# Performance work log

Measured on AMD Instinct MI355X. Metric: run time of the kernel, lower is better.

The kernel has to match this reference:

```python
import jax, jax.numpy as jnp
import numpy as np

NUM_NODES = 2048
NODE_DIM = 64
BATCH = 16


def setup_inputs() -> dict:
    key = jax.random.key(0)
    ks = jax.random.split(key, 8)
    s = 1.0 / np.sqrt(NODE_DIM)
    return {
        "x_temp": jax.random.normal(ks[0], (BATCH, NUM_NODES, NODE_DIM), jnp.float32),
        "node_emb": jax.random.normal(ks[1], (NUM_NODES, NODE_DIM), jnp.float32),
        "w1_w": jax.random.uniform(ks[2], (NODE_DIM, NODE_DIM), jnp.float32, -s, s),
        "w1_b": jax.random.uniform(ks[3], (NODE_DIM,), jnp.float32, -s, s),
        "w2_w": jax.random.uniform(ks[4], (NODE_DIM, NODE_DIM), jnp.float32, -s, s),
        "w2_b": jax.random.uniform(ks[5], (NODE_DIM,), jnp.float32, -s, s),
        "wp_w": jax.random.uniform(ks[6], (1, NODE_DIM), jnp.float32, -s, s),
        "wp_b": jax.random.uniform(ks[7], (1,), jnp.float32, -s, s),
    }


def reference(x_temp, node_emb, w1_w, w1_b, w2_w, w2_b, wp_w, wp_b):
    # static bilinear adjacency over learned node embeddings: [N, N]
    node_1 = node_emb @ w1_w.T + w1_b
    node_2 = node_emb @ w2_w.T + w2_b
    adj_base = jax.nn.relu(node_1 @ node_2.T)
    # dynamic similarity from temporal states: [B, N, N]
    dyn = jnp.einsum("bnd,bmd->bnm", x_temp, x_temp)
    # directional (wind-like) antisymmetric bias: v_i - v_j
    v = x_temp @ wp_w.T + wp_b  # [B, N, 1]
    directional_bias = v - jnp.swapaxes(v, 1, 2)  # [B, N, N]
    adj = adj_base[None, :, :] + dyn + directional_bias
    return jax.nn.softmax(adj, axis=-1)
```

## Files before the change

### kernel.cpp

```cpp
#include <hip/hip_runtime.h>

#define BB 16
#define NN 2048
#define DD 64
#define MC 128
#define NCH (NN / MC)
#define TM 8

#define FW 8
#define FT 16


typedef __bf16 bf16x8 __attribute__((ext_vector_type(8)));
typedef float f32x4 __attribute__((ext_vector_type(4)));
typedef int i32x4 __attribute__((ext_vector_type(4)));
typedef unsigned short u16x8 __attribute__((ext_vector_type(8)));

#define MFMA16 __builtin_amdgcn_mfma_f32_16x16x32_bf16

__device__ inline unsigned short f2bf(float f) {
  unsigned u = __float_as_uint(f);
  unsigned r = u + 0x7FFFu + ((u >> 16) & 1u);
  return (unsigned short)(r >> 16);
}
__device__ inline float bf2f(unsigned short h) {
  return __uint_as_float(((unsigned)h) << 16);
}
__device__ inline bf16x8 ldfrag(const unsigned short* p) {
  i32x4 v = *reinterpret_cast<const i32x4*>(p);
  return __builtin_bit_cast(bf16x8, v);
}

__global__ __launch_bounds__(256) void prep_nodes(
    const float* __restrict__ emb, const float* __restrict__ w1w,
    const float* __restrict__ w1b, const float* __restrict__ w2w,
    const float* __restrict__ w2b, float* __restrict__ n1f,
    float* __restrict__ n2f, unsigned short* __restrict__ n1hi,
    unsigned short* __restrict__ n1lo, unsigned short* __restrict__ n2hi,
    unsigned short* __restrict__ n2lo, int wantbf)
{
  __shared__ float wl[2][DD][DD + 1];
  int t = threadIdx.x;
  for (int i = t; i < DD * DD; i += 256) {
    wl[0][i >> 6][i & 63] = w1w[i];
    wl[1][i >> 6][i & 63] = w2w[i];
  }
  __syncthreads();
  int g = blockIdx.x * 256 + t;
  int which = (g >= NN * DD) ? 1 : 0;
  int idx = which ? g - NN * DD : g;
  int n = idx >> 6, d = idx & 63;
  const float* e = emb + (size_t)n * DD;
  float s = which ? w2b[d] : w1b[d];
  #pragma unroll
  for (int k = 0; k < DD; ++k) s += e[k] * wl[which][d][k];
  (which ? n2f : n1f)[idx] = s;
  if (wantbf) {
    unsigned short hi = f2bf(s);
    unsigned short lo = f2bf(s - bf2f(hi));
    int ti = (n >> 4) * 1024 + (d >> 3) * 128 + (n & 15) * 8 + (d & 7);
    (which ? n2hi : n1hi)[ti] = hi;
    (which ? n2lo : n1lo)[ti] = lo;
  }
}

__global__ __launch_bounds__(256) void prep_x(
    const float* __restrict__ x, unsigned short* __restrict__ xhi,
    unsigned short* __restrict__ xlo)
{
  int G = blockIdx.x * 256 + threadIdx.x;
  int b = G >> 14;
  int rem = G & 16383;
  int tile = rem >> 7, oct = (rem >> 4) & 7, m = rem & 15;
  const float* src = x + ((size_t)b * NN + tile * 16 + m) * DD + oct * 8;
  float4 x0 = *(const float4*)src;
  float4 x1 = *(const float4*)(src + 4);
  u16x8 hv, lv;
  hv[0] = f2bf(x0.x); lv[0] = f2bf(x0.x - bf2f(hv[0]));
  hv[1] = f2bf(x0.y); lv[1] = f2bf(x0.y - bf2f(hv[1]));
  hv[2] = f2bf(x0.z); lv[2] = f2bf(x0.z - bf2f(hv[2]));
  hv[3] = f2bf(x0.w); lv[3] = f2bf(x0.w - bf2f(hv[3]));
  hv[4] = f2bf(x1.x); lv[4] = f2bf(x1.x - bf2f(hv[4]));
  hv[5] = f2bf(x1.y); lv[5] = f2bf(x1.y - bf2f(hv[5]));
  hv[6] = f2bf(x1.z); lv[6] = f2bf(x1.z - bf2f(hv[6]));
  hv[7] = f2bf(x1.w); lv[7] = f2bf(x1.w - bf2f(hv[7]));
  *(u16x8*)&xhi[(size_t)G * 8] = hv;
  *(u16x8*)&xlo[(size_t)G * 8] = lv;
}

__global__ __launch_bounds__(256) void prep_v(
    const float* __restrict__ x, const float* __restrict__ wpw,
    const float* __restrict__ wpb, float* __restrict__ v)
{
  int g = blockIdx.x * 256 + threadIdx.x;
  const float* xr = x + (size_t)g * DD;
  float s = wpb[0];
  #pragma unroll
  for (int kq = 0; kq < DD / 4; ++kq) {
    float4 q = *(const float4*)&xr[kq * 4];
    float4 w = *(const float4*)&wpw[kq * 4];
    s += q.x * w.x + q.y * w.y + q.z * w.z + q.w * w.w;
  }
  v[g] = s;
}

__global__ __launch_bounds__(256) void base_mfma(
    const unsigned short* __restrict__ n1hi, const unsigned short* __restrict__ n1lo,
    const unsigned short* __restrict__ n2hi, const unsigned short* __restrict__ n2lo,
    float* __restrict__ base)
{
  int t = threadIdx.x, lane = t & 63, w = t >> 6;
  int q = lane >> 4, m = lane & 15;
  int n0 = blockIdx.x * 16;
  int cw = blockIdx.y * 256 + w * 64;
  int la8 = lane * 8;
  bf16x8 ah0 = ldfrag(n1hi + n0 * 64 + la8), ah1 = ldfrag(n1hi + n0 * 64 + 512 + la8);
  bf16x8 al0 = ldfrag(n1lo + n0 * 64 + la8), al1 = ldfrag(n1lo + n0 * 64 + 512 + la8);
  #pragma unroll
  for (int tt = 0; tt < 4; ++tt) {
    int c0 = cw + tt * 16;
    bf16x8 bh0 = ldfrag(n2hi + c0 * 64 + la8), bh1 = ldfrag(n2hi + c0 * 64 + 512 + la8);
    bf16x8 bl0 = ldfrag(n2lo + c0 * 64 + la8), bl1 = ldfrag(n2lo + c0 * 64 + 512 + la8);
    f32x4 a = {0.f, 0.f, 0.f, 0.f};
    f32x4 bq = {0.f, 0.f, 0.f, 0.f};
    a = MFMA16(ah0, bh0, a, 0, 0, 0);
    a = MFMA16(ah1, bh1, a, 0, 0, 0);
    bq = MFMA16(ah0, bl0, bq, 0, 0, 0);
    bq = MFMA16(ah1, bl1, bq, 0, 0, 0);
    bq = MFMA16(al0, bh0, bq, 0, 0, 0);
    bq = MFMA16(al1, bh1, bq, 0, 0, 0);
    #pragma unroll
    for (int r = 0; r < 4; ++r)
      base[(size_t)(n0 + q * 4 + r) * NN + c0 + m] = fmaxf(a[r] + bq[r], 0.f);
  }
}

__global__ __launch_bounds__(512, 4) void fused_mfma(
    const unsigned short* __restrict__ xhi, const unsigned short* __restrict__ xlo,
    const float* __restrict__ base, const float* __restrict__ vv,
    float* __restrict__ out)
{
  __shared__ float redm[FW][16];
  __shared__ float reds[FW][16];
  int t = threadIdx.x, lane = t & 63, w = t >> 6;
  int q = lane >> 4, m = lane & 15;
  int b = blockIdx.y, n0 = blockIdx.x * 16, cw = w * (FT * 16);
  size_t xb = (size_t)b * NN * DD;
  int la8 = lane * 8;

  const unsigned short* ah = xhi + xb + n0 * 64;
  const unsigned short* al = xlo + xb + n0 * 64;
  bf16x8 ah0 = ldfrag(ah + la8), ah1 = ldfrag(ah + 512 + la8);
  bf16x8 al0 = ldfrag(al + la8), al1 = ldfrag(al + 512 + la8);

  float vrow[4];
  #pragma unroll
  for (int r = 0; r < 4; ++r) vrow[r] = vv[b * NN + n0 + q * 4 + r];

  f32x4 acc[FT];
  #pragma unroll
  for (int tt = 0; tt < FT; ++tt) {
    int c0 = cw + tt * 16;
    const unsigned short* bh = xhi + xb + c0 * 64;
    const unsigned short* bl = xlo + xb + c0 * 64;
    bf16x8 bh0 = ldfrag(bh + la8), bh1 = ldfrag(bh + 512 + la8);
    bf16x8 bl0 = ldfrag(bl + la8), bl1 = ldfrag(bl + 512 + la8);
    f32x4 a = {0.f, 0.f, 0.f, 0.f};
    f32x4 bq = {0.f, 0.f, 0.f, 0.f};
    a = MFMA16(ah0, bh0, a, 0, 0, 0);
    a = MFMA16(ah1, bh1, a, 0, 0, 0);
    bq = MFMA16(ah0, bl0, bq, 0, 0, 0);
    bq = MFMA16(ah1, bl1, bq, 0, 0, 0);
    bq = MFMA16(al0, bh0, bq, 0, 0, 0);
    bq = MFMA16(al1, bh1, bq, 0, 0, 0);
    float vc = vv[b * NN + c0 + m];
    #pragma unroll
    for (int r = 0; r < 4; ++r)
      a[r] += bq[r] + base[(size_t)(n0 + q * 4 + r) * NN + c0 + m] + vrow[r] - vc;
    acc[tt] = a;
  }

  float mx[4];
  #pragma unroll
  for (int r = 0; r < 4; ++r) mx[r] = acc[0][r];
  #pragma unroll
  for (int tt = 1; tt < FT; ++tt)
    #pragma unroll
    for (int r = 0; r < 4; ++r) mx[r] = fmaxf(mx[r], acc[tt][r]);
  #pragma unroll
  for (int off = 8; off >= 1; off >>= 1)
    #pragma unroll
    for (int r = 0; r < 4; ++r) mx[r] = fmaxf(mx[r], __shfl_xor(mx[r], off, 64));
  if (m == 0) {
    #pragma unroll
    for (int r = 0; r < 4; ++r) redm[w][q * 4 + r] = mx[r];
  }
  __syncthreads();
  float mrow[4], sm[4];
  #pragma unroll
  for (int r = 0; r < 4; ++r) {
    int rr = q * 4 + r;
    float mv = redm[0][rr];
    #pragma unroll
    for (int ww = 1; ww < FW; ++ww) mv = fmaxf(mv, redm[ww][rr]);
    mrow[r] = mv;
    sm[r] = 0.f;
  }
  #pragma unroll
  for (int tt = 0; tt < FT; ++tt)
    #pragma unroll
    for (int r = 0; r < 4; ++r) {
      float e = __expf(acc[tt][r] - mrow[r]);
      acc[tt][r] = e;
      sm[r] += e;
    }
  #pragma unroll
  for (int off = 8; off >= 1; off >>= 1)
    #pragma unroll
    for (int r = 0; r < 4; ++r) sm[r] += __shfl_xor(sm[r], off, 64);
  if (m == 0) {
    #pragma unroll
    for (int r = 0; r < 4; ++r) reds[w][q * 4 + r] = sm[r];
  }
  __syncthreads();
  float inv[4];
  #pragma unroll
  for (int r = 0; r < 4; ++r) {
    int rr = q * 4 + r;
    float sv = reds[0][rr];
    #pragma unroll
    for (int ww = 1; ww < FW; ++ww) sv += reds[ww][rr];
    inv[r] = 1.f / sv;
  }
  #pragma unroll
  for (int tt = 0; tt < FT; ++tt) {
    int c = cw + tt * 16 + m;
    #pragma unroll
    for (int r = 0; r < 4; ++r)
      out[((size_t)b * NN + n0 + q * 4 + r) * NN + c] = acc[tt][r] * inv[r];
  }
}

__global__ __launch_bounds__(256) void fused_fallback(
    const float* __restrict__ x, const float* __restrict__ node1,
    const float* __restrict__ node2, const float* __restrict__ vv,
    float* __restrict__ out)
{
  __shared__ float xr[TM][DD];
  __shared__ float n1r[TM][DD];
  __shared__ float colbuf[2][DD / 2][MC + 1];
  __shared__ float redm[4][4];
  __shared__ float reds[4][4];

  int t = threadIdx.x;
  int b = blockIdx.y;
  int n0 = blockIdx.x * TM;
  int mloc = t & (MC - 1);
  int grp = t >> 7;
  int r0 = grp * 4;

  for (int i = t; i < TM * DD; i += 256) {
    xr[i >> 6][i & 63] = x[((size_t)b * NN + n0) * DD + i];
    n1r[i >> 6][i & 63] = node1[(size_t)n0 * DD + i];
  }
  float vrow[4];
  #pragma unroll
  for (int r = 0; r < 4; ++r) vrow[r] = vv[b * NN + n0 + r0 + r];

  float acc[4][NCH];

  #pragma unroll
  for (int c = 0; c < NCH; ++c) {
    float dacc[4] = {0.f, 0.f, 0.f, 0.f};
    float bacc[4] = {0.f, 0.f, 0.f, 0.f};
    #pragma unroll
    for (int h = 0; h < 2; ++h) {
      __syncthreads();
      #pragma unroll
      for (int i = 0; i < 8; ++i) {
        int f = i * 256 + t;
        int arr = f >> 10;
        int ff = f & 1023;
        int mm = ff >> 3, kq = ff & 7;
        const float* src = arr
            ? node2 + (size_t)(c * MC + mm) * DD + h * 32 + kq * 4
            : x + ((size_t)b * NN + c * MC + mm) * DD + h * 32 + kq * 4;
        float4 qv = *(const float4*)src;
        colbuf[arr][kq * 4 + 0][mm] = qv.x;
        colbuf[arr][kq * 4 + 1][mm] = qv.y;
        colbuf[arr][kq * 4 + 2][mm] = qv.z;
        colbuf[arr][kq * 4 + 3][mm] = qv.w;
      }
      __syncthreads();
      #pragma unroll
      for (int kb = 0; kb < 8; ++kb) {
        float ra[4][4], rb[4][4];
        #pragma unroll
        for (int r = 0; r < 4; ++r) {
          float4 qx = *(const float4*)&xr[r0 + r][h * 32 + kb * 4];
          ra[r][0] = qx.x; ra[r][1] = qx.y; ra[r][2] = qx.z; ra[r][3] = qx.w;
          float4 qn = *(const float4*)&n1r[r0 + r][h * 32 + kb * 4];
          rb[r][0] = qn.x; rb[r][1] = qn.y; rb[r][2] = qn.z; rb[r][3] = qn.w;
        }
        #pragma unroll
        for (int kk = 0; kk < 4; ++kk) {
          float cx = colbuf[0][kb * 4 + kk][mloc];
          float cn = colbuf[1][kb * 4 + kk][mloc];
          #pragma unroll
          for (int r = 0; r < 4; ++r) {
            dacc[r] += ra[r][kk] * cx;
            bacc[r] += rb[r][kk] * cn;
          }
        }
      }
    }
    float vc = vv[b * NN + c * MC + mloc];
    #pragma unroll
    for (int r = 0; r < 4; ++r)
      acc[r][c] = dacc[r] + vrow[r] - vc + fmaxf(bacc[r], 0.f);
  }

  float pm[4];
  #pragma unroll
  for (int r = 0; r < 4; ++r) {
    float mv = acc[r][0];
    #pragma unroll
    for (int c = 1; c < NCH; ++c) mv = fmaxf(mv, acc[r][c]);
    #pragma unroll
    for (int off = 32; off >= 1; off >>= 1)
      mv = fmaxf(mv, __shfl_xor(mv, off, 64));
    pm[r] = mv;
  }
  int w = t >> 6;
  if ((t & 63) == 0) {
    #pragma unroll
    for (int r = 0; r < 4; ++r) redm[w][r] = pm[r];
  }
  __syncthreads();
  float mrow[4], ps[4];
  #pragma unroll
  for (int r = 0; r < 4; ++r) {
    mrow[r] = fmaxf(redm[grp * 2][r], redm[grp * 2 + 1][r]);
    ps[r] = 0.f;
  }
  #pragma unroll
  for (int c = 0; c < NCH; ++c)
    #pragma unroll
    for (int r = 0; r < 4; ++r) {
      float e = __expf(acc[r][c] - mrow[r]);
      acc[r][c] = e;
      ps[r] += e;
    }
  #pragma unroll
  for (int r = 0; r < 4; ++r)
    #pragma unroll
    for (int off = 32; off >= 1; off >>= 1)
      ps[r] += __shfl_xor(ps[r], off, 64);
  if ((t & 63) == 0) {
    #pragma unroll
    for (int r = 0; r < 4; ++r) reds[w][r] = ps[r];
  }
  __syncthreads();
  float inv[4];
  #pragma unroll
  for (int r = 0; r < 4; ++r)
    inv[r] = 1.f / (reds[grp * 2][r] + reds[grp * 2 + 1][r]);
  #pragma unroll
  for (int c = 0; c < NCH; ++c)
    #pragma unroll
    for (int r = 0; r < 4; ++r)
      out[((size_t)b * NN + n0 + r0 + r) * NN + c * MC + mloc] = acc[r][c] * inv[r];
}

extern "C" void kernel_launch(void* const* d_in, const int* in_sizes, int n_in,
                              void* d_out, int out_size, void* d_ws, size_t ws_size,
                              hipStream_t stream)
{
  const float* x   = (const float*)d_in[0];
  const float* emb = (const float*)d_in[1];
  const float* w1w = (const float*)d_in[2];
  const float* w1b = (const float*)d_in[3];
  const float* w2w = (const float*)d_in[4];
  const float* w2b = (const float*)d_in[5];
  const float* wpw = (const float*)d_in[6];
  const float* wpb = (const float*)d_in[7];
  float* out = (float*)d_out;

  float* wsf   = (float*)d_ws;
  float* node1 = wsf;
  float* node2 = wsf + (size_t)NN * DD;
  float* v     = wsf + (size_t)2 * NN * DD;
  float* base  = wsf + (size_t)2 * NN * DD + (size_t)BB * NN;
  unsigned short* bfb = (unsigned short*)(base + (size_t)NN * NN);
  unsigned short* xhi = bfb;
  unsigned short* xlo = xhi + (size_t)BB * NN * DD;
  unsigned short* n1hi = xlo + (size_t)BB * NN * DD;
  unsigned short* n1lo = n1hi + (size_t)NN * DD;
  unsigned short* n2hi = n1lo + (size_t)NN * DD;
  unsigned short* n2lo = n2hi + (size_t)NN * DD;

  size_t need_mfma = ((size_t)2 * NN * DD + (size_t)BB * NN + (size_t)NN * NN) * 4
                   + ((size_t)2 * BB * NN * DD + (size_t)4 * NN * DD) * 2;
  bool big = ws_size >= need_mfma;

  prep_nodes<<<2 * NN * DD / 256, 256, 0, stream>>>(
      emb, w1w, w1b, w2w, w2b, node1, node2, n1hi, n1lo, n2hi, n2lo, big ? 1 : 0);
  prep_v<<<BB * NN / 256, 256, 0, stream>>>(x, wpw, wpb, v);

  if (big) {
    prep_x<<<BB * NN * DD / 8 / 256, 256, 0, stream>>>(x, xhi, xlo);
    dim3 bgrid(NN / 16, 8);
    base_mfma<<<bgrid, 256, 0, stream>>>(n1hi, n1lo, n2hi, n2lo, base);
    dim3 grid(NN / 16, BB);
    fused_mfma<<<grid, 512, 0, stream>>>(xhi, xlo, base, v, out);
  } else {
    dim3 grid(NN / TM, BB);
    fused_fallback<<<grid, 256, 0, stream>>>(x, node1, node2, v, out);
  }
}
```

Before: 389.6 us.

## Store base adjacency in MFMA fragment layout, merge prep kernels, swizzle block order

```diff
diff --git a/kernel.cpp b/kernel.cpp
--- a/kernel.cpp
+++ b/kernel.cpp
@@ -31,87 +31,84 @@
   return __builtin_bit_cast(bf16x8, v);
 }
 
-__global__ __launch_bounds__(256) void prep_nodes(
-    const float* __restrict__ emb, const float* __restrict__ w1w,
-    const float* __restrict__ w1b, const float* __restrict__ w2w,
-    const float* __restrict__ w2b, float* __restrict__ n1f,
-    float* __restrict__ n2f, unsigned short* __restrict__ n1hi,
-    unsigned short* __restrict__ n1lo, unsigned short* __restrict__ n2hi,
-    unsigned short* __restrict__ n2lo, int wantbf)
+__global__ __launch_bounds__(256) void prep_all(
+    const float* __restrict__ x, const float* __restrict__ emb,
+    const float* __restrict__ w1w, const float* __restrict__ w1b,
+    const float* __restrict__ w2w, const float* __restrict__ w2b,
+    const float* __restrict__ wpw, const float* __restrict__ wpb,
+    float* __restrict__ n1f, float* __restrict__ n2f,
+    unsigned short* __restrict__ n1hi, unsigned short* __restrict__ n1lo,
+    unsigned short* __restrict__ n2hi, unsigned short* __restrict__ n2lo,
+    unsigned short* __restrict__ xhi, unsigned short* __restrict__ xlo,
+    float* __restrict__ v, int wantbf)
 {
   __shared__ float wl[2][DD][DD + 1];
-  int t = threadIdx.x;
-  for (int i = t; i < DD * DD; i += 256) {
-    wl[0][i >> 6][i & 63] = w1w[i];
-    wl[1][i >> 6][i & 63] = w2w[i];
-  }
-  __syncthreads();
-  int g = blockIdx.x * 256 + t;
-  int which = (g >= NN * DD) ? 1 : 0;
-  int idx = which ? g - NN * DD : g;
-  int n = idx >> 6, d = idx & 63;
-  const float* e = emb + (size_t)n * DD;
-  float s = which ? w2b[d] : w1b[d];
-  #pragma unroll
-  for (int k = 0; k < DD; ++k) s += e[k] * wl[which][d][k];
-  (which ? n2f : n1f)[idx] = s;
-  if (wantbf) {
-    unsigned short hi = f2bf(s);
-    unsigned short lo = f2bf(s - bf2f(hi));
-    int ti = (n >> 4) * 1024 + (d >> 3) * 128 + (n & 15) * 8 + (d & 7);
-    (which ? n2hi : n1hi)[ti] = hi;
-    (which ? n2lo : n1lo)[ti] = lo;
-  }
-}
-
-__global__ __launch_bounds__(256) void prep_x(
-    const float* __restrict__ x, unsigned short* __restrict__ xhi,
-    unsigned short* __restrict__ xlo)
-{
-  int G = blockIdx.x * 256 + threadIdx.x;
-  int b = G >> 14;
-  int rem = G & 16383;
-  int tile = rem >> 7, oct = (rem >> 4) & 7, m = rem & 15;
-  const float* src = x + ((size_t)b * NN + tile * 16 + m) * DD + oct * 8;
-  float4 x0 = *(const float4*)src;
-  float4 x1 = *(const float4*)(src + 4);
-  u16x8 hv, lv;
-  hv[0] = f2bf(x0.x); lv[0] = f2bf(x0.x - bf2f(hv[0]));
-  hv[1] = f2bf(x0.y); lv[1] = f2bf(x0.y - bf2f(hv[1]));
-  hv[2] = f2bf(x0.z); lv[2] = f2bf(x0.z - bf2f(hv[2]));
-  hv[3] = f2bf(x0.w); lv[3] = f2bf(x0.w - bf2f(hv[3]));
-  hv[4] = f2bf(x1.x); lv[4] = f2bf(x1.x - bf2f(hv[4]));
-  hv[5] = f2bf(x1.y); lv[5] = f2bf(x1.y - bf2f(hv[5]));
-  hv[6] = f2bf(x1.z); lv[6] = f2bf(x1.z - bf2f(hv[6]));
-  hv[7] = f2bf(x1.w); lv[7] = f2bf(x1.w - bf2f(hv[7]));
-  *(u16x8*)&xhi[(size_t)G * 8] = hv;
-  *(u16x8*)&xlo[(size_t)G * 8] = lv;
-}
-
-__global__ __launch_bounds__(256) void prep_v(
-    const float* __restrict__ x, const float* __restrict__ wpw,
-    const float* __restrict__ wpb, float* __restrict__ v)
-{
-  int g = blockIdx.x * 256 + threadIdx.x;
-  const float* xr = x + (size_t)g * DD;
-  float s = wpb[0];
-  #pragma unroll
-  for (int kq = 0; kq < DD / 4; ++kq) {
-    float4 q = *(const float4*)&xr[kq * 4];
-    float4 w = *(const float4*)&wpw[kq * 4];
-    s += q.x * w.x + q.y * w.y + q.z * w.z + q.w * w.w;
-  }
-  v[g] = s;
+  int t = threadIdx.x, bx = blockIdx.x;
+
+  if (bx < 1024) {
+    for (int i = t; i < DD * DD; i += 256) {
+      wl[0][i >> 6][i & 63] = w1w[i];
+      wl[1][i >> 6][i & 63] = w2w[i];
+    }
+    __syncthreads();
+    int g = bx * 256 + t;
+    int which = (g >= NN * DD) ? 1 : 0;
+    int idx = which ? g - NN * DD : g;
+    int n = idx >> 6, d = idx & 63;
+    const float* e = emb + (size_t)n * DD;
+    float s = which ? w2b[d] : w1b[d];
+    #pragma unroll
+    for (int k = 0; k < DD; ++k) s += e[k] * wl[which][d][k];
+    (which ? n2f : n1f)[idx] = s;
+    if (wantbf) {
+      unsigned short hi = f2bf(s);
+      unsigned short lo = f2bf(s - bf2f(hi));
+      int ti = (n >> 4) * 1024 + (d >> 3) * 128 + (n & 15) * 8 + (d & 7);
+      (which ? n2hi : n1hi)[ti] = hi;
+      (which ? n2lo : n1lo)[ti] = lo;
+    }
+  } else if (bx < 2048) {
+    if (!wantbf) return;
+    int G = (bx - 1024) * 256 + t;
+    int b = G >> 14;
+    int rem = G & 16383;
+    int tile = rem >> 7, oct = (rem >> 4) & 7, m = rem & 15;
+    const float* src = x + ((size_t)b * NN + tile * 16 + m) * DD + oct * 8;
+    float4 x0 = *(const float4*)src;
+    float4 x1 = *(const float4*)(src + 4);
+    u16x8 hv, lv;
+    hv[0] = f2bf(x0.x); lv[0] = f2bf(x0.x - bf2f(hv[0]));
+    hv[1] = f2bf(x0.y); lv[1] = f2bf(x0.y - bf2f(hv[1]));
+    hv[2] = f2bf(x0.z); lv[2] = f2bf(x0.z - bf2f(hv[2]));
+    hv[3] = f2bf(x0.w); lv[3] = f2bf(x0.w - bf2f(hv[3]));
+    hv[4] = f2bf(x1.x); lv[4] = f2bf(x1.x - bf2f(hv[4]));
+    hv[5] = f2bf(x1.y); lv[5] = f2bf(x1.y - bf2f(hv[5]));
+    hv[6] = f2bf(x1.z); lv[6] = f2bf(x1.z - bf2f(hv[6]));
+    hv[7] = f2bf(x1.w); lv[7] = f2bf(x1.w - bf2f(hv[7]));
+    *(u16x8*)&xhi[(size_t)G * 8] = hv;
+    *(u16x8*)&xlo[(size_t)G * 8] = lv;
+  } else {
+    int g = (bx - 2048) * 256 + t;
+    const float* xr = x + (size_t)g * DD;
+    float s = wpb[0];
+    #pragma unroll
+    for (int kq = 0; kq < DD / 4; ++kq) {
+      float4 q = *(const float4*)&xr[kq * 4];
+      float4 w = *(const float4*)&wpw[kq * 4];
+      s += q.x * w.x + q.y * w.y + q.z * w.z + q.w * w.w;
+    }
+    v[g] = s;
+  }
 }
 
 __global__ __launch_bounds__(256) void base_mfma(
     const unsigned short* __restrict__ n1hi, const unsigned short* __restrict__ n1lo,
     const unsigned short* __restrict__ n2hi, const unsigned short* __restrict__ n2lo,
-    float* __restrict__ base)
+    float* __restrict__ baset)
 {
   int t = threadIdx.x, lane = t & 63, w = t >> 6;
-  int q = lane >> 4, m = lane & 15;
-  int n0 = blockIdx.x * 16;
+  int rt = blockIdx.x;
+  int n0 = rt * 16;
   int cw = blockIdx.y * 256 + w * 64;
   int la8 = lane * 8;
   bf16x8 ah0 = ldfrag(n1hi + n0 * 64 + la8), ah1 = ldfrag(n1hi + n0 * 64 + 512 + la8);
@@ -129,22 +126,27 @@
     bq = MFMA16(ah1, bl1, bq, 0, 0, 0);
     bq = MFMA16(al0, bh0, bq, 0, 0, 0);
     bq = MFMA16(al1, bh1, bq, 0, 0, 0);
-    #pragma unroll
-    for (int r = 0; r < 4; ++r)
-      base[(size_t)(n0 + q * 4 + r) * NN + c0 + m] = fmaxf(a[r] + bq[r], 0.f);
+    f32x4 r4;
+    #pragma unroll
+    for (int r = 0; r < 4; ++r) r4[r] = fmaxf(a[r] + bq[r], 0.f);
+    *(f32x4*)&baset[(((size_t)rt * 128 + (c0 >> 4)) * 64 + lane) * 4] = r4;
   }
 }
 
 __global__ __launch_bounds__(512, 4) void fused_mfma(
     const unsigned short* __restrict__ xhi, const unsigned short* __restrict__ xlo,
-    const float* __restrict__ base, const float* __restrict__ vv,
+    const float* __restrict__ baset, const float* __restrict__ vv,
     float* __restrict__ out)
 {
   __shared__ float redm[FW][16];
   __shared__ float reds[FW][16];
   int t = threadIdx.x, lane = t & 63, w = t >> 6;
   int q = lane >> 4, m = lane & 15;
-  int b = blockIdx.y, n0 = blockIdx.x * 16, cw = w * (FT * 16);
+  int bid = blockIdx.x;
+  int swz = (bid & 7) * 256 + (bid >> 3);
+  int b = swz >> 7;
+  int n0 = (swz & 127) * 16;
+  int cw = w * (FT * 16);
   size_t xb = (size_t)b * NN * DD;
   int la8 = lane * 8;
 
@@ -165,6 +167,7 @@
     const unsigned short* bl = xlo + xb + c0 * 64;
     bf16x8 bh0 = ldfrag(bh + la8), bh1 = ldfrag(bh + 512 + la8);
     bf16x8 bl0 = ldfrag(bl + la8), bl1 = ldfrag(bl + 512 + la8);
+    f32x4 bs = *(const f32x4*)&baset[(((size_t)(n0 >> 4) * 128 + (c0 >> 4)) * 64 + lane) * 4];
     f32x4 a = {0.f, 0.f, 0.f, 0.f};
     f32x4 bq = {0.f, 0.f, 0.f, 0.f};
     a = MFMA16(ah0, bh0, a, 0, 0, 0);
@@ -176,7 +179,7 @@
     float vc = vv[b * NN + c0 + m];
     #pragma unroll
     for (int r = 0; r < 4; ++r)
-      a[r] += bq[r] + base[(size_t)(n0 + q * 4 + r) * NN + c0 + m] + vrow[r] - vc;
+      a[r] += bq[r] + bs[r] + vrow[r] - vc;
     acc[tt] = a;
   }
 
@@ -390,8 +393,8 @@
   float* node1 = wsf;
   float* node2 = wsf + (size_t)NN * DD;
   float* v     = wsf + (size_t)2 * NN * DD;
-  float* base  = wsf + (size_t)2 * NN * DD + (size_t)BB * NN;
-  unsigned short* bfb = (unsigned short*)(base + (size_t)NN * NN);
+  float* baset = wsf + (size_t)2 * NN * DD + (size_t)BB * NN;
+  unsigned short* bfb = (unsigned short*)(baset + (size_t)NN * NN);
   unsigned short* xhi = bfb;
   unsigned short* xlo = xhi + (size_t)BB * NN * DD;
   unsigned short* n1hi = xlo + (size_t)BB * NN * DD;
@@ -403,16 +406,14 @@
                    + ((size_t)2 * BB * NN * DD + (size_t)4 * NN * DD) * 2;
   bool big = ws_size >= need_mfma;
 
-  prep_nodes<<<2 * NN * DD / 256, 256, 0, stream>>>(
-      emb, w1w, w1b, w2w, w2b, node1, node2, n1hi, n1lo, n2hi, n2lo, big ? 1 : 0);
-  prep_v<<<BB * NN / 256, 256, 0, stream>>>(x, wpw, wpb, v);
+  prep_all<<<2176, 256, 0, stream>>>(
+      x, emb, w1w, w1b, w2w, w2b, wpw, wpb,
+      node1, node2, n1hi, n1lo, n2hi, n2lo, xhi, xlo, v, big ? 1 : 0);
 
   if (big) {
-    prep_x<<<BB * NN * DD / 8 / 256, 256, 0, stream>>>(x, xhi, xlo);
     dim3 bgrid(NN / 16, 8);
-    base_mfma<<<bgrid, 256, 0, stream>>>(n1hi, n1lo, n2hi, n2lo, base);
-    dim3 grid(NN / 16, BB);
-    fused_mfma<<<grid, 512, 0, stream>>>(xhi, xlo, base, v, out);
+    base_mfma<<<bgrid, 256, 0, stream>>>(n1hi, n1lo, n2hi, n2lo, baset);
+    fused_mfma<<<NN / 16 * BB, 512, 0, stream>>>(xhi, xlo, baset, v, out);
   } else {
     dim3 grid(NN / TM, BB);
     fused_fallback<<<grid, 256, 0, stream>>>(x, node1, node2, v, out);
```

Measured after the change: 338.9 us. -13.0%, faster.
